# Performance work log

Measured on AMD Instinct MI355X. Metric: run time of the kernel, lower is better.

Reference implementation:

```python
import jax, jax.numpy as jnp
import numpy as np

N_SRC = 50000
N_DST = 50000
E = 800000
D = 128
K = 8  # args.k: number of randomly sampled neighbors


def setup_inputs() -> dict:
    key = jax.random.key(0)
    k1, k2, k3, k4, k5, k6 = jax.random.split(key, 6)
    h_src = jax.random.normal(k1, (N_SRC, D), dtype=jnp.float32)
    h_dst = jax.random.normal(k2, (N_DST, D), dtype=jnp.float32)
    unif = jax.random.uniform(k3, (N_DST, K), dtype=jnp.float32)
    src_idx = jax.random.randint(k4, (E,), 0, N_SRC, dtype=jnp.int32)
    dst_idx = jnp.sort(jax.random.randint(k5, (E,), 0, N_DST, dtype=jnp.int32))
    category = jax.random.randint(k6, (N_SRC,), 0, 50, dtype=jnp.int32)
    return {"h_src": h_src, "h_dst": h_dst, "unif": unif,
            "src_idx": src_idx, "dst_idx": dst_idx, "category": category}


def _forward(h_src, h_dst, unif, src_idx, dst_idx, category):
    n_src = h_src.shape[0]
    n_dst = h_dst.shape[0]
    e = src_idx.shape[0]
    ones = jnp.ones((e,), dtype=h_src.dtype)

    # src-side symmetric norm: feat_src * out_deg^-0.5
    out_deg = jax.ops.segment_sum(ones, src_idx, num_segments=n_src)
    out_norm = jnp.clip(out_deg, 1.0, None) ** -0.5
    feat_src = h_src * out_norm[:, None]

    # mailbox gather: message per edge m_e = feat_src[src_e]  -> [E, D]
    msg = feat_src[src_idx]

    # in-degrees and full segment-sum reduction
    in_deg = jax.ops.segment_sum(ones, dst_idx, num_segments=n_dst)
    full_sum = jax.ops.segment_sum(msg, dst_idx, num_segments=n_dst)  # [N_dst, D]

    # random neighbor subsampling with replacement (dst_idx is sorted):
    # node n owns edges [ptr[n], ptr[n]+deg[n]); pick K offsets via floor(u*deg)
    deg_i = in_deg.astype(jnp.int32)
    ptr = jnp.searchsorted(dst_idx, jnp.arange(n_dst, dtype=jnp.int32), side="left").astype(jnp.int32)
    off = jnp.floor(unif * in_deg[:, None]).astype(jnp.int32)
    off = jnp.minimum(off, jnp.maximum(deg_i[:, None] - 1, 0))  # guard u==1 / deg==0
    eid = jnp.clip(ptr[:, None] + off, 0, e - 1)                # [N_dst, K]
    samp_sum = msg[eid].sum(axis=1)                              # [N_dst, D]

    # bucket escape hatch: any incoming category == -1 -> sum everything
    neg_in = jax.ops.segment_sum((category[src_idx] == -1).astype(jnp.int32),
                                 dst_idx, num_segments=n_dst)
    use_full = (deg_i <= K) | (neg_in > 0)
    rst = jnp.where(use_full[:, None], full_sum, samp_sum)

    # dst-side norm: rst * in_deg^-0.5
    in_norm = jnp.clip(in_deg, 1.0, None) ** -0.5
    return rst * in_norm[:, None]


def reference(h_src, h_dst, unif, src_idx, dst_idx, category):
    return _forward(h_src, h_dst, unif, src_idx, dst_idx, category)
```

## Files before the change

kernel.cpp:

```cpp
#include <hip/hip_runtime.h>

#define N_SRC 50000
#define N_DST 50000
#define E_CNT 800000
#define D 128
#define K 8

#define HIST_BLOCKS 128
#define HIST_THREADS 512
#define PTR_BLOCKS ((N_DST + 1 + HIST_THREADS - 1) / HIST_THREADS)
#define HALF 25000
#define HWORDS (HALF / 2)
#define SLAB_WORDS (N_SRC / 2)
#define NCHUNK (E_CNT / 4)


__device__ __forceinline__ int lower_bound_dst(const int* __restrict__ d, int key) {
    int lo = 0, hi = E_CNT;
    while (lo < hi) {
        int mid = (lo + hi) >> 1;
        if (d[mid] < key) lo = mid + 1; else hi = mid;
    }
    return lo;
}

__global__ __launch_bounds__(HIST_THREADS)
void count_ptr_kernel(const int* __restrict__ src_idx,
                      const int* __restrict__ dst_idx,
                      const int* __restrict__ category,
                      const float* __restrict__ unif,
                      unsigned* __restrict__ slab,
                      int* __restrict__ blockflag,
                      int* __restrict__ ptr,
                      float* __restrict__ in_norm,
                      int* __restrict__ samp,
                      unsigned char* __restrict__ degs) {
    if (blockIdx.x < HIST_BLOCKS) {
        __shared__ unsigned hist[HWORDS];
        __shared__ int blkneg;
        if (threadIdx.x == 0) blkneg = 0;
        const int4* s4 = (const int4*)src_idx;
        unsigned* myslab = slab + (size_t)blockIdx.x * SLAB_WORDS;
        int negf = 0;

        for (int pass = 0; pass < 2; ++pass) {
            int base = pass * HALF;
            for (int j = threadIdx.x; j < HWORDS; j += HIST_THREADS) hist[j] = 0;
            __syncthreads();

            for (int c = blockIdx.x * HIST_THREADS + threadIdx.x; c < NCHUNK;
                 c += HIST_BLOCKS * HIST_THREADS) {
                int4 s = s4[c];
                int r;
                r = s.x - base; if ((unsigned)r < HALF) atomicAdd(&hist[r >> 1], 1u << ((r & 1) * 16));
                r = s.y - base; if ((unsigned)r < HALF) atomicAdd(&hist[r >> 1], 1u << ((r & 1) * 16));
                r = s.z - base; if ((unsigned)r < HALF) atomicAdd(&hist[r >> 1], 1u << ((r & 1) * 16));
                r = s.w - base; if ((unsigned)r < HALF) atomicAdd(&hist[r >> 1], 1u << ((r & 1) * 16));
                if (pass == 0) {
                    negf |= (category[s.x] == -1) | (category[s.y] == -1) |
                            (category[s.z] == -1) | (category[s.w] == -1);
                }
            }
            __syncthreads();

            for (int j = threadIdx.x; j < HWORDS; j += HIST_THREADS)
                myslab[pass * HWORDS + j] = hist[j];
            __syncthreads();
        }
        if (negf) atomicOr(&blkneg, 1);
        __syncthreads();
        if (threadIdx.x == 0) blockflag[blockIdx.x] = blkneg;
    } else {
        int n = (blockIdx.x - HIST_BLOCKS) * HIST_THREADS + threadIdx.x;
        int lane = threadIdx.x & 63;
        int lo = 0;
        if (n <= N_DST) {
            lo = lower_bound_dst(dst_idx, n);
            ptr[n] = lo;
        }
        int hi = __shfl_down(lo, 1, 64);
        if (lane == 63 && n < N_DST) hi = lower_bound_dst(dst_idx, n + 1);
        if (n >= N_DST) return;

        int deg = hi - lo;
        in_norm[n] = rsqrtf((float)max(deg, 1));
        int m = min(deg, K);
        degs[n] = (unsigned char)m;

        int ids[K];
        if (deg > K) {
            const float4* u4 = (const float4*)(unif + (size_t)n * K);
            float4 ua = u4[0], ub = u4[1];
            float uu[K] = {ua.x, ua.y, ua.z, ua.w, ub.x, ub.y, ub.z, ub.w};
            #pragma unroll
            for (int k = 0; k < K; ++k) {
                int off = (int)floorf(uu[k] * (float)deg);
                if (off > deg - 1) off = deg - 1;
                if (off < 0) off = 0;
                int eid = lo + off;
                if (eid > E_CNT - 1) eid = E_CNT - 1;
                ids[k] = src_idx[eid];
            }
        } else {
            #pragma unroll
            for (int k = 0; k < K; ++k) {
                int eid = lo + k;
                if (eid > E_CNT - 1) eid = E_CNT - 1;
                ids[k] = src_idx[eid];
            }
        }
        int4* sp = (int4*)(samp + (size_t)n * K);
        sp[0] = make_int4(ids[0], ids[1], ids[2], ids[3]);
        sp[1] = make_int4(ids[4], ids[5], ids[6], ids[7]);
    }
}

__global__ __launch_bounds__(256)
void reduce_norm_kernel(const unsigned* __restrict__ slab,
                        const int* __restrict__ blockflag,
                        float* __restrict__ out_norm,
                        int* __restrict__ any_neg) {
    int w = blockIdx.x * 256 + threadIdx.x;
    if (blockIdx.x == 0 && threadIdx.x == 0) {
        int f = 0;
        #pragma unroll 16
        for (int b = 0; b < HIST_BLOCKS; ++b) f |= blockflag[b];
        *any_neg = f;
    }
    if (w >= SLAB_WORDS) return;
    int lo = 0, hi = 0;
    #pragma unroll 16
    for (int b = 0; b < HIST_BLOCKS; ++b) {
        unsigned v = slab[(size_t)b * SLAB_WORDS + w];
        lo += (int)(v & 0xffffu);
        hi += (int)(v >> 16);
    }
    int pass = w / HWORDS;
    int j = w - pass * HWORDS;
    float2 r = make_float2(rsqrtf((float)max(lo, 1)), rsqrtf((float)max(hi, 1)));
    ((float2*)out_norm)[pass * HWORDS + j] = r;
}

__global__ void gather_kernel(const float* __restrict__ h_src,
                              const int* __restrict__ src_idx,
                              const int* __restrict__ category,
                              const float* __restrict__ out_norm,
                              const int* __restrict__ any_neg,
                              const int* __restrict__ ptr,
                              const float* __restrict__ in_norm,
                              const int* __restrict__ samp,
                              const unsigned char* __restrict__ degs,
                              float* __restrict__ out) {
    int wave = (blockIdx.x * blockDim.x + threadIdx.x) >> 6;
    int lane = threadIdx.x & 63;
    int sub = lane & 31;
    int hbase = lane & 32;
    int n = wave * 2 + (lane >> 5);
    if (n >= N_DST) return;

    int m = degs[n];
    float inr = in_norm[n];

    const float4* h4 = (const float4*)h_src;
    float4 acc = make_float4(0.f, 0.f, 0.f, 0.f);

    bool escape = false;
    if (*any_neg) {
        int p = ptr[n];
        int deg = ptr[n + 1] - p;
        for (int i = 0; i < deg && !escape; ++i)
            escape = (category[src_idx[p + i]] == -1);
        if (escape && deg > K) {
            for (int i = 0; i < deg; ++i) {
                int s = src_idx[p + i];
                float nrm = out_norm[s];
                float4 v = h4[(size_t)s * 32 + sub];
                acc.x += v.x * nrm;
                acc.y += v.y * nrm;
                acc.z += v.z * nrm;
                acc.w += v.w * nrm;
            }
        } else {
            escape = false;
        }
    }

    if (!escape) {
        int s_k = 0;
        float n_k = 0.f;
        if (sub < K) {
            s_k = samp[(size_t)n * K + sub];
            n_k = (sub < m) ? out_norm[s_k] : 0.f;
        }
        #pragma unroll
        for (int k = 0; k < K; ++k) {
            int s = __shfl(s_k, hbase + k, 64);
            float nrm = __shfl(n_k, hbase + k, 64);
            float4 v = h4[(size_t)s * 32 + sub];
            acc.x += v.x * nrm;
            acc.y += v.y * nrm;
            acc.z += v.z * nrm;
            acc.w += v.w * nrm;
        }
    }

    float4 r;
    r.x = acc.x * inr;
    r.y = acc.y * inr;
    r.z = acc.z * inr;
    r.w = acc.w * inr;
    ((float4*)out)[(size_t)n * 32 + sub] = r;
}

extern "C" void kernel_launch(void* const* d_in, const int* in_sizes, int n_in,
                              void* d_out, int out_size, void* d_ws, size_t ws_size,
                              hipStream_t stream) {
    const float* h_src   = (const float*)d_in[0];
    const float* unif    = (const float*)d_in[2];
    const int* src_idx   = (const int*)d_in[3];
    const int* dst_idx   = (const int*)d_in[4];
    const int* category  = (const int*)d_in[5];
    float* out = (float*)d_out;

    unsigned* slab  = (unsigned*)d_ws;
    int* blockflag  = (int*)(slab + (size_t)HIST_BLOCKS * SLAB_WORDS);
    int* any_neg    = blockflag + HIST_BLOCKS;
    int* ptr        = any_neg + 4;
    float* out_norm = (float*)(ptr + N_DST + 4);
    float* in_norm  = out_norm + N_SRC;
    int* samp       = (int*)(in_norm + N_DST);
    unsigned char* degs = (unsigned char*)(samp + (size_t)N_DST * K);


    count_ptr_kernel<<<HIST_BLOCKS + PTR_BLOCKS, HIST_THREADS, 0, stream>>>(
        src_idx, dst_idx, category, unif, slab, blockflag, ptr, in_norm, samp, degs);

    reduce_norm_kernel<<<(SLAB_WORDS + 255) / 256, 256, 0, stream>>>(
        slab, blockflag, out_norm, any_neg);

    {
        int threads = 256;
        int blocks = (N_DST + 7) / 8;
        gather_kernel<<<blocks, threads, 0, stream>>>(h_src, src_idx, category,
                                                      out_norm, any_neg, ptr,
                                                      in_norm, samp, degs, out);
    }
}
```

Before: 134.1 us.

## Pack source-degree histogram into 8-bit counters in one pass with fewer blocks

Replaces the two-pass 16-bit packed shared-memory histogram with a single pass using four 8-bit counters per word, so the full source range fits in shared memory at once. Halves the histogram block count, shrinking the per-block slab and the reduction work. Source indices are read once instead of twice. Risks counter overflow if any source gets more than 255 edges within one block's share.

```diff
diff --git a/kernel.cpp b/kernel.cpp
--- a/kernel.cpp
+++ b/kernel.cpp
@@ -6,12 +6,10 @@
 #define D 128
 #define K 8
 
-#define HIST_BLOCKS 128
+#define HIST_BLOCKS 64
 #define HIST_THREADS 512
 #define PTR_BLOCKS ((N_DST + 1 + HIST_THREADS - 1) / HIST_THREADS)
-#define HALF 25000
-#define HWORDS (HALF / 2)
-#define SLAB_WORDS (N_SRC / 2)
+#define HWORDS ((N_SRC + 3) / 4)
 #define NCHUNK (E_CNT / 4)
 
 
@@ -40,33 +38,27 @@
         __shared__ int blkneg;
         if (threadIdx.x == 0) blkneg = 0;
         const int4* s4 = (const int4*)src_idx;
-        unsigned* myslab = slab + (size_t)blockIdx.x * SLAB_WORDS;
+        unsigned* myslab = slab + (size_t)blockIdx.x * HWORDS;
         int negf = 0;
 
-        for (int pass = 0; pass < 2; ++pass) {
-            int base = pass * HALF;
-            for (int j = threadIdx.x; j < HWORDS; j += HIST_THREADS) hist[j] = 0;
-            __syncthreads();
-
-            for (int c = blockIdx.x * HIST_THREADS + threadIdx.x; c < NCHUNK;
-                 c += HIST_BLOCKS * HIST_THREADS) {
-                int4 s = s4[c];
-                int r;
-                r = s.x - base; if ((unsigned)r < HALF) atomicAdd(&hist[r >> 1], 1u << ((r & 1) * 16));
-                r = s.y - base; if ((unsigned)r < HALF) atomicAdd(&hist[r >> 1], 1u << ((r & 1) * 16));
-                r = s.z - base; if ((unsigned)r < HALF) atomicAdd(&hist[r >> 1], 1u << ((r & 1) * 16));
-                r = s.w - base; if ((unsigned)r < HALF) atomicAdd(&hist[r >> 1], 1u << ((r & 1) * 16));
-                if (pass == 0) {
-                    negf |= (category[s.x] == -1) | (category[s.y] == -1) |
-                            (category[s.z] == -1) | (category[s.w] == -1);
-                }
-            }
-            __syncthreads();
-
-            for (int j = threadIdx.x; j < HWORDS; j += HIST_THREADS)
-                myslab[pass * HWORDS + j] = hist[j];
-            __syncthreads();
-        }
+        for (int j = threadIdx.x; j < HWORDS; j += HIST_THREADS) hist[j] = 0;
+        __syncthreads();
+
+        for (int c = blockIdx.x * HIST_THREADS + threadIdx.x; c < NCHUNK;
+             c += HIST_BLOCKS * HIST_THREADS) {
+            int4 s = s4[c];
+            atomicAdd(&hist[s.x >> 2], 1u << ((s.x & 3) * 8));
+            atomicAdd(&hist[s.y >> 2], 1u << ((s.y & 3) * 8));
+            atomicAdd(&hist[s.z >> 2], 1u << ((s.z & 3) * 8));
+            atomicAdd(&hist[s.w >> 2], 1u << ((s.w & 3) * 8));
+            negf |= (category[s.x] == -1) | (category[s.y] == -1) |
+                    (category[s.z] == -1) | (category[s.w] == -1);
+        }
+        __syncthreads();
+
+        for (int j = threadIdx.x; j < HWORDS; j += HIST_THREADS)
+            myslab[j] = hist[j];
+
         if (negf) atomicOr(&blkneg, 1);
         __syncthreads();
         if (threadIdx.x == 0) blockflag[blockIdx.x] = blkneg;
@@ -127,18 +119,19 @@
         for (int b = 0; b < HIST_BLOCKS; ++b) f |= blockflag[b];
         *any_neg = f;
     }
-    if (w >= SLAB_WORDS) return;
-    int lo = 0, hi = 0;
+    if (w >= HWORDS) return;
+    int c0 = 0, c1 = 0, c2 = 0, c3 = 0;
     #pragma unroll 16
     for (int b = 0; b < HIST_BLOCKS; ++b) {
-        unsigned v = slab[(size_t)b * SLAB_WORDS + w];
-        lo += (int)(v & 0xffffu);
-        hi += (int)(v >> 16);
-    }
-    int pass = w / HWORDS;
-    int j = w - pass * HWORDS;
-    float2 r = make_float2(rsqrtf((float)max(lo, 1)), rsqrtf((float)max(hi, 1)));
-    ((float2*)out_norm)[pass * HWORDS + j] = r;
+        unsigned v = slab[(size_t)b * HWORDS + w];
+        c0 += (int)(v & 0xffu);
+        c1 += (int)((v >> 8) & 0xffu);
+        c2 += (int)((v >> 16) & 0xffu);
+        c3 += (int)(v >> 24);
+    }
+    float4 r = make_float4(rsqrtf((float)max(c0, 1)), rsqrtf((float)max(c1, 1)),
+                           rsqrtf((float)max(c2, 1)), rsqrtf((float)max(c3, 1)));
+    ((float4*)out_norm)[w] = r;
 }
 
 __global__ void gather_kernel(const float* __restrict__ h_src,
@@ -223,7 +216,7 @@
     float* out = (float*)d_out;
 
     unsigned* slab  = (unsigned*)d_ws;
-    int* blockflag  = (int*)(slab + (size_t)HIST_BLOCKS * SLAB_WORDS);
+    int* blockflag  = (int*)(slab + (size_t)HIST_BLOCKS * HWORDS);
     int* any_neg    = blockflag + HIST_BLOCKS;
     int* ptr        = any_neg + 4;
     float* out_norm = (float*)(ptr + N_DST + 4);
@@ -235,7 +228,7 @@
     count_ptr_kernel<<<HIST_BLOCKS + PTR_BLOCKS, HIST_THREADS, 0, stream>>>(
         src_idx, dst_idx, category, unif, slab, blockflag, ptr, in_norm, samp, degs);
 
-    reduce_norm_kernel<<<(SLAB_WORDS + 255) / 256, 256, 0, stream>>>(
+    reduce_norm_kernel<<<(HWORDS + 255) / 256, 256, 0, stream>>>(
         slab, blockflag, out_norm, any_neg);
 
     {
```

Result: faster. 131.1 us (-2.3%).
